# Performance work log

Hardware: AMD Instinct MI355X
Metric: run time of the kernel (lower is better)

The kernel has to match this reference:

```python
import jax, jax.numpy as jnp
import numpy as np

B, D, E, K = 8192, 1024, 8, 5  # batch, in_dim, num_size_classes, num_depth_classes
H = max(64, D)                 # hidden = max(64, in_dim)
EPS = 1e-8


def ordinal_logits_to_probs(logits, num_classes):
    # logits: [B, K-1] cumulative ordinal logits -> [B, K] class probs
    q = jax.nn.sigmoid(logits)
    probs = jnp.concatenate(
        [1.0 - q[:, :1], q[:, :-1] - q[:, 1:], q[:, -1:]], axis=1
    )  # [B, K]
    probs = jnp.clip(probs, EPS)
    return probs / jnp.clip(probs.sum(axis=1, keepdims=True), EPS)


def setup_inputs() -> dict:
    key = jax.random.key(0)
    kx, ks, k1, k2 = jax.random.split(key, 4)
    x = jax.random.normal(kx, (B, D), dtype=jnp.float32)
    size_idx = jax.random.randint(ks, (B,), 0, E, dtype=jnp.int64)
    # per-expert 2-layer MLP params: Linear(D,H) -> ReLU -> Linear(H,K-1)
    W1 = jax.random.normal(k1, (E, D, H), dtype=jnp.float32) / np.sqrt(D)
    b1 = jnp.zeros((E, H), dtype=jnp.float32)
    W2 = jax.random.normal(k2, (E, H, K - 1), dtype=jnp.float32) / np.sqrt(H)
    b2 = jnp.zeros((E, K - 1), dtype=jnp.float32)
    return {"x": x, "size_idx": size_idx, "W1": W1, "b1": b1, "W2": W2, "b2": b2}


def reference(x, size_idx, W1, b1, W2, b2):
    # Hard routing: each token gets the output of expert size_idx[b].
    # Dense all-expert compute + per-token select (same math as mask/gather/scatter,
    # dropout is inference-mode identity).
    h = jax.nn.relu(jnp.einsum('bd,edh->beh', x, W1) + b1)      # [B, E, H]
    all_logits = jnp.einsum('beh,ehk->bek', h, W2) + b2          # [B, E, K-1]
    idx = size_idx.astype(jnp.int32)[:, None, None]              # [B, 1, 1]
    logits = jnp.take_along_axis(all_logits, idx, axis=1)[:, 0]  # [B, K-1]
    probs = ordinal_logits_to_probs(logits, K)                   # [B, K]
    return logits, probs
```

## Files before the change

### kernel.cpp

```cpp
#include <hip/hip_runtime.h>
#include <cstdint>
#include <cstddef>

#define Bn 8192
#define Dn 1024
#define Hn 1024
#define En 8
#define MT 128
#define MTILES (PERM_N / MT)
#define PERM_N (Bn + En * MT)
#define NB 16

#define NXB 4096
#define NWB 2048
#define XB0 1
#define WB0 (XB0 + NXB)
#define TOTB (WB0 + NWB)

typedef unsigned short u16;
typedef __bf16 bf16x8 __attribute__((ext_vector_type(8)));
typedef float f32x4 __attribute__((ext_vector_type(4)));
typedef unsigned short ushort8 __attribute__((ext_vector_type(8)));

__device__ __forceinline__ u16 f2bf(float f) {
  unsigned int u = __float_as_uint(f);
  unsigned int r = u + 0x7fffu + ((u >> 16) & 1u);
  return (u16)(r >> 16);
}

__device__ __forceinline__ void gld16(const void* g, void* l) {
  __builtin_amdgcn_global_load_lds(
      (const __attribute__((address_space(1))) void*)g,
      (__attribute__((address_space(3))) void*)l, 16, 0, 0);
}

#define PIPE_BARRIER_VM8() do {                    \
    asm volatile("" ::: "memory");                 \
    __builtin_amdgcn_s_waitcnt(0x0F78);            \
    __builtin_amdgcn_s_barrier();                  \
    asm volatile("" ::: "memory");                 \
  } while (0)
#define PIPE_BARRIER_VM4() do {                    \
    asm volatile("" ::: "memory");                 \
    __builtin_amdgcn_s_waitcnt(0x0F74);            \
    __builtin_amdgcn_s_barrier();                  \
    asm volatile("" ::: "memory");                 \
  } while (0)
#define PIPE_BARRIER_VM0() do {                    \
    asm volatile("" ::: "memory");                 \
    __builtin_amdgcn_s_waitcnt(0x0F70);            \
    __builtin_amdgcn_s_barrier();                  \
    asm volatile("" ::: "memory");                 \
  } while (0)

__global__ __launch_bounds__(256) void prep_k(
    const float* __restrict__ x, const int* __restrict__ sidx,
    const float* __restrict__ W1,
    u16* __restrict__ xb, u16* __restrict__ w1t,
    int* __restrict__ off, int* __restrict__ perm) {
  int bid = blockIdx.x;
  int t = threadIdx.x;

  if (bid == 0) {
    __shared__ int hist[4][En];
    __shared__ int base[4][En];
    __shared__ int eoff[En + 1];
    int wv = t >> 6;
    if (t < 4 * En) ((int*)hist)[t] = 0;
#pragma unroll
    for (int i = 0; i < PERM_N / 256; i++) perm[t + i * 256] = -1;
    __syncthreads();
    int e32[32], r32[32];
#pragma unroll
    for (int i = 0; i < 32; i++) {
      int e = sidx[t + i * 256];
      e32[i] = e;
      r32[i] = atomicAdd(&hist[wv][e], 1);
    }
    __syncthreads();
    if (t < En) {
      int s = 0;
      for (int w = 0; w < 4; w++) { base[w][t] = s; s += hist[w][t]; }
      hist[0][t] = s;
    }
    __syncthreads();
    if (t == 0) {
      int o = 0;
      for (int e = 0; e < En; e++) {
        eoff[e] = o; off[e] = o;
        o += (hist[0][e] + MT - 1) & ~(MT - 1);
      }
      eoff[En] = o; off[En] = o;
    }
    __syncthreads();
#pragma unroll
    for (int i = 0; i < 32; i++) {
      int e = e32[i];
      perm[eoff[e] + base[wv][e] + r32[i]] = t + i * 256;
    }
  } else if (bid < WB0) {
    size_t idx = ((size_t)(bid - XB0) * 256 + t) * 8;
    const float* src = x + idx;
    float4 a = *(const float4*)src;
    float4 b = *(const float4*)(src + 4);
    ushort8 o;
    o[0] = f2bf(a.x); o[1] = f2bf(a.y); o[2] = f2bf(a.z); o[3] = f2bf(a.w);
    o[4] = f2bf(b.x); o[5] = f2bf(b.y); o[6] = f2bf(b.z); o[7] = f2bf(b.w);
    *(ushort8*)(xb + idx) = o;
  } else {
    __shared__ float tile[64][65];
    int wb = bid - WB0;
    int e = wb >> 8;
    int k0 = ((wb >> 4) & 15) * 64;
    int n0 = (wb & 15) * 64;
    int c4 = (t & 15) * 4;
    int r0 = t >> 4;
    const float* src = W1 + ((size_t)e << 20) + (size_t)k0 * Hn + n0;
#pragma unroll
    for (int i = 0; i < 4; i++) {
      int r = r0 + i * 16;
      float4 v = *(const float4*)(src + (size_t)r * Hn + c4);
      tile[r][c4 + 0] = v.x; tile[r][c4 + 1] = v.y;
      tile[r][c4 + 2] = v.z; tile[r][c4 + 3] = v.w;
    }
    __syncthreads();
    int kb = t & 7;
    int h0 = t >> 3;
    u16* dstE = w1t + ((size_t)e << 20);
#pragma unroll
    for (int i = 0; i < 2; i++) {
      int hl = h0 + i * 32;
      int gh = n0 + hl;
      ushort8 o;
#pragma unroll
      for (int j = 0; j < 8; j++) o[j] = f2bf(tile[kb * 8 + j][hl]);
      *(ushort8*)(dstE + (size_t)gh * Dn + k0 + kb * 8) = o;
    }
  }
}

__global__ __launch_bounds__(256) void gemm_k(
    const u16* __restrict__ xb, const u16* __restrict__ w1t,
    const float* __restrict__ b1, const float* __restrict__ w2,
    const int* __restrict__ off, const int* __restrict__ perm,
    float* __restrict__ partials) {
  __shared__ u16 As[4][4096];
  __shared__ u16 Bs[4][4096];

  int n0 = blockIdx.x * 128;
  int row0 = blockIdx.y * MT;
  if (row0 >= off[En]) return;
  int e = 0;
  while (row0 >= off[e + 1]) e++;

  int tid = threadIdx.x;
  int lane = tid & 63, w = tid >> 6;
  int wm = w >> 1, wn = w & 1;

  int srow = lane >> 2;
  int slot = lane & 3;
  int scol = (slot ^ ((srow >> 1) & 3)) * 8;
  const u16* aG[2]; const u16* bG[2];
  int lOff[2];
#pragma unroll
  for (int j = 0; j < 2; j++) {
    int rl = 32 * w + 16 * j + srow;
    int tok = perm[row0 + rl];
    if (tok < 0) tok = 0;
    aG[j] = xb + ((size_t)tok << 10) + scol;
    bG[j] = w1t + ((size_t)e << 20) + (size_t)(n0 + rl) * Dn + scol;
    lOff[j] = (32 * w + 16 * j) * 32;
  }

  f32x4 acc[4][4];
#pragma unroll
  for (int i = 0; i < 4; i++)
#pragma unroll
    for (int j = 0; j < 4; j++)
      acc[i][j] = (f32x4){0.f, 0.f, 0.f, 0.f};

  int fr = lane & 15;
  int qf = lane >> 4;
  int qs = (qf ^ ((fr >> 1) & 3)) * 8;
  int offA[4], offB[4];
#pragma unroll
  for (int i = 0; i < 4; i++)
    offA[i] = (wm * 64 + i * 16 + fr) * 32 + qs;
#pragma unroll
  for (int j = 0; j < 4; j++)
    offB[j] = (wn * 64 + j * 16 + fr) * 32 + qs;

#define ISSUE_STAGE(st) do {                                          \
    int _s = (st) & 3;                                                \
    int _ko = (st) * 32;                                              \
    gld16(aG[0] + _ko, (u16*)As[_s] + lOff[0]);                       \
    gld16(aG[1] + _ko, (u16*)As[_s] + lOff[1]);                       \
    gld16(bG[0] + _ko, (u16*)Bs[_s] + lOff[0]);                       \
    gld16(bG[1] + _ko, (u16*)Bs[_s] + lOff[1]);                       \
  } while (0)

#define COMPUTE_STAGE(st) do {                                        \
    const u16* Ab = (const u16*)As[(st) & 3];                         \
    const u16* Bb = (const u16*)Bs[(st) & 3];                         \
    bf16x8 af[4], bfr[4];                                             \
    _Pragma("unroll")                                                 \
    for (int ii = 0; ii < 4; ii++) af[ii] = *(const bf16x8*)(Ab + offA[ii]); \
    _Pragma("unroll")                                                 \
    for (int jj = 0; jj < 4; jj++) bfr[jj] = *(const bf16x8*)(Bb + offB[jj]); \
    _Pragma("unroll")                                                 \
    for (int ii = 0; ii < 4; ii++)                                    \
      _Pragma("unroll")                                               \
      for (int jj = 0; jj < 4; jj++)                                  \
        acc[ii][jj] = __builtin_amdgcn_mfma_f32_16x16x32_bf16(af[ii], bfr[jj], acc[ii][jj], 0, 0, 0); \
  } while (0)

  ISSUE_STAGE(0);
  ISSUE_STAGE(1);
  ISSUE_STAGE(2);

#pragma unroll
  for (int i = 0; i < 30; i++) {
    PIPE_BARRIER_VM8();
    if (i + 3 < 32) ISSUE_STAGE(i + 3);
    COMPUTE_STAGE(i);
  }
  PIPE_BARRIER_VM4();
  COMPUTE_STAGE(30);
  PIPE_BARRIER_VM0();
  COMPUTE_STAGE(31);

#undef ISSUE_STAGE
#undef COMPUTE_STAGE

  int fq = lane >> 4;
  float4 w2v[4]; float b1v[4];
#pragma unroll
  for (int j = 0; j < 4; j++) {
    int col = n0 + wn * 64 + j * 16 + fr;
    w2v[j] = *(const float4*)(w2 + ((size_t)e * Hn + col) * 4);
    b1v[j] = b1[(size_t)e * Hn + col];
  }
  int chunk = blockIdx.x * 2 + wn;
#pragma unroll
  for (int i = 0; i < 4; i++) {
    int rbase = wm * 64 + i * 16 + fq * 4;
#pragma unroll
    for (int r = 0; r < 4; r++) {
      float s0 = 0.f, s1 = 0.f, s2 = 0.f, s3 = 0.f;
#pragma unroll
      for (int j = 0; j < 4; j++) {
        float h = acc[i][j][r] + b1v[j];
        h = fmaxf(h, 0.f);
        s0 = fmaf(h, w2v[j].x, s0);
        s1 = fmaf(h, w2v[j].y, s1);
        s2 = fmaf(h, w2v[j].z, s2);
        s3 = fmaf(h, w2v[j].w, s3);
      }
#pragma unroll
      for (int m = 1; m < 16; m <<= 1) {
        s0 += __shfl_xor(s0, m);
        s1 += __shfl_xor(s1, m);
        s2 += __shfl_xor(s2, m);
        s3 += __shfl_xor(s3, m);
      }
      if (fr == 0) {
        int row = row0 + rbase + r;
        *(float4*)(partials + ((size_t)row * NB + chunk) * 4) =
            make_float4(s0, s1, s2, s3);
      }
    }
  }
}

__global__ void probs_k(const float* __restrict__ partials,
                        const int* __restrict__ perm, const int* __restrict__ off,
                        const int* __restrict__ sidx, const float* __restrict__ b2,
                        float* __restrict__ out) {
  int p = blockIdx.x * blockDim.x + threadIdx.x;
  if (p >= off[En]) return;
  int tok = perm[p];
  if (tok < 0) return;
  int e = sidx[tok];
  float s0 = 0.f, s1 = 0.f, s2 = 0.f, s3 = 0.f;
#pragma unroll
  for (int nb = 0; nb < NB; nb++) {
    float4 v = *(const float4*)(partials + ((size_t)p * NB + nb) * 4);
    s0 += v.x; s1 += v.y; s2 += v.z; s3 += v.w;
  }
  float l0 = s0 + b2[e * 4 + 0];
  float l1 = s1 + b2[e * 4 + 1];
  float l2 = s2 + b2[e * 4 + 2];
  float l3 = s3 + b2[e * 4 + 3];
  out[tok * 4 + 0] = l0; out[tok * 4 + 1] = l1;
  out[tok * 4 + 2] = l2; out[tok * 4 + 3] = l3;
  float q0 = 1.f / (1.f + expf(-l0));
  float q1 = 1.f / (1.f + expf(-l1));
  float q2 = 1.f / (1.f + expf(-l2));
  float q3 = 1.f / (1.f + expf(-l3));
  const float eps = 1e-8f;
  float p0 = fmaxf(1.f - q0, eps);
  float p1 = fmaxf(q0 - q1, eps);
  float p2 = fmaxf(q1 - q2, eps);
  float p3 = fmaxf(q2 - q3, eps);
  float p4 = fmaxf(q3, eps);
  float s = p0 + p1 + p2 + p3 + p4;
  float inv = 1.f / fmaxf(s, eps);
  float* pr = out + (size_t)Bn * 4 + (size_t)tok * 5;
  pr[0] = p0 * inv; pr[1] = p1 * inv; pr[2] = p2 * inv;
  pr[3] = p3 * inv; pr[4] = p4 * inv;
}

extern "C" void kernel_launch(void* const* d_in, const int* in_sizes, int n_in,
                              void* d_out, int out_size, void* d_ws, size_t ws_size,
                              hipStream_t stream) {
  const float* x  = (const float*)d_in[0];
  const int* sidx = (const int*)d_in[1];
  const float* W1 = (const float*)d_in[2];
  const float* b1 = (const float*)d_in[3];
  const float* W2 = (const float*)d_in[4];
  const float* b2 = (const float*)d_in[5];
  float* out = (float*)d_out;

  uint8_t* w = (uint8_t*)d_ws;
  int* off  = (int*)(w + 64);
  int* perm = (int*)(w + 512);
  u16* xb      = (u16*)(w + 40960);
  u16* w1t     = (u16*)(w + 40960 + 16777216);
  float* parts = (float*)(w + 40960 + 2 * 16777216);

  prep_k<<<TOTB, 256, 0, stream>>>(x, sidx, W1, xb, w1t, off, perm);
  gemm_k<<<dim3(Hn / 128, MTILES), 256, 0, stream>>>(xb, w1t, b1, W2, off, perm, parts);
  probs_k<<<(PERM_N + 255) / 256, 256, 0, stream>>>(parts, perm, off, sidx, b2, out);
}
```

Measured before the change: 175.4 us.

## Fuse x bf16 conversion into GEMM A-tile loads with register-staged double buffering

```diff
diff --git a/kernel.cpp b/kernel.cpp
--- a/kernel.cpp
+++ b/kernel.cpp
@@ -7,15 +7,10 @@
 #define Hn 1024
 #define En 8
 #define MT 128
+#define PERM_N (Bn + En * MT)
 #define MTILES (PERM_N / MT)
-#define PERM_N (Bn + En * MT)
 #define NB 16
-
-#define NXB 4096
 #define NWB 2048
-#define XB0 1
-#define WB0 (XB0 + NXB)
-#define TOTB (WB0 + NWB)
 
 typedef unsigned short u16;
 typedef __bf16 bf16x8 __attribute__((ext_vector_type(8)));
@@ -34,30 +29,9 @@
       (__attribute__((address_space(3))) void*)l, 16, 0, 0);
 }
 
-#define PIPE_BARRIER_VM8() do {                    \
-    asm volatile("" ::: "memory");                 \
-    __builtin_amdgcn_s_waitcnt(0x0F78);            \
-    __builtin_amdgcn_s_barrier();                  \
-    asm volatile("" ::: "memory");                 \
-  } while (0)
-#define PIPE_BARRIER_VM4() do {                    \
-    asm volatile("" ::: "memory");                 \
-    __builtin_amdgcn_s_waitcnt(0x0F74);            \
-    __builtin_amdgcn_s_barrier();                  \
-    asm volatile("" ::: "memory");                 \
-  } while (0)
-#define PIPE_BARRIER_VM0() do {                    \
-    asm volatile("" ::: "memory");                 \
-    __builtin_amdgcn_s_waitcnt(0x0F70);            \
-    __builtin_amdgcn_s_barrier();                  \
-    asm volatile("" ::: "memory");                 \
-  } while (0)
-
 __global__ __launch_bounds__(256) void prep_k(
-    const float* __restrict__ x, const int* __restrict__ sidx,
-    const float* __restrict__ W1,
-    u16* __restrict__ xb, u16* __restrict__ w1t,
-    int* __restrict__ off, int* __restrict__ perm) {
+    const int* __restrict__ sidx, const float* __restrict__ W1,
+    u16* __restrict__ w1t, int* __restrict__ off, int* __restrict__ perm) {
   int bid = blockIdx.x;
   int t = threadIdx.x;
 
@@ -98,18 +72,9 @@
       int e = e32[i];
       perm[eoff[e] + base[wv][e] + r32[i]] = t + i * 256;
     }
-  } else if (bid < WB0) {
-    size_t idx = ((size_t)(bid - XB0) * 256 + t) * 8;
-    const float* src = x + idx;
-    float4 a = *(const float4*)src;
-    float4 b = *(const float4*)(src + 4);
-    ushort8 o;
-    o[0] = f2bf(a.x); o[1] = f2bf(a.y); o[2] = f2bf(a.z); o[3] = f2bf(a.w);
-    o[4] = f2bf(b.x); o[5] = f2bf(b.y); o[6] = f2bf(b.z); o[7] = f2bf(b.w);
-    *(ushort8*)(xb + idx) = o;
   } else {
     __shared__ float tile[64][65];
-    int wb = bid - WB0;
+    int wb = bid - 1;
     int e = wb >> 8;
     int k0 = ((wb >> 4) & 15) * 64;
     int n0 = (wb & 15) * 64;
@@ -124,28 +89,27 @@
       tile[r][c4 + 2] = v.z; tile[r][c4 + 3] = v.w;
     }
     __syncthreads();
-    int kb = t & 7;
-    int h0 = t >> 3;
-    u16* dstE = w1t + ((size_t)e << 20);
-#pragma unroll
-    for (int i = 0; i < 2; i++) {
-      int hl = h0 + i * 32;
-      int gh = n0 + hl;
-      ushort8 o;
-#pragma unroll
-      for (int j = 0; j < 8; j++) o[j] = f2bf(tile[kb * 8 + j][hl]);
-      *(ushort8*)(dstE + (size_t)gh * Dn + k0 + kb * 8) = o;
+    u16* dst = w1t + ((size_t)e << 20) + (size_t)n0 * Dn + k0;
+#pragma unroll
+    for (int i = 0; i < 4; i++) {
+      int h = r0 + i * 16;
+      ushort4 o;
+      o.x = f2bf(tile[c4 + 0][h]);
+      o.y = f2bf(tile[c4 + 1][h]);
+      o.z = f2bf(tile[c4 + 2][h]);
+      o.w = f2bf(tile[c4 + 3][h]);
+      *(ushort4*)(dst + (size_t)h * Dn + c4) = o;
     }
   }
 }
 
 __global__ __launch_bounds__(256) void gemm_k(
-    const u16* __restrict__ xb, const u16* __restrict__ w1t,
+    const float* __restrict__ x, const u16* __restrict__ w1t,
     const float* __restrict__ b1, const float* __restrict__ w2,
     const int* __restrict__ off, const int* __restrict__ perm,
     float* __restrict__ partials) {
-  __shared__ u16 As[4][4096];
-  __shared__ u16 Bs[4][4096];
+  __shared__ u16 As[2][4096];
+  __shared__ u16 Bs[2][4096];
 
   int n0 = blockIdx.x * 128;
   int row0 = blockIdx.y * MT;
@@ -160,16 +124,19 @@
   int srow = lane >> 2;
   int slot = lane & 3;
   int scol = (slot ^ ((srow >> 1) & 3)) * 8;
-  const u16* aG[2]; const u16* bG[2];
+  const float* aF[2];
+  const u16* bG[2];
   int lOff[2];
+  int aW[2];
 #pragma unroll
   for (int j = 0; j < 2; j++) {
     int rl = 32 * w + 16 * j + srow;
     int tok = perm[row0 + rl];
     if (tok < 0) tok = 0;
-    aG[j] = xb + ((size_t)tok << 10) + scol;
+    aF[j] = x + ((size_t)tok << 10) + scol;
     bG[j] = w1t + ((size_t)e << 20) + (size_t)(n0 + rl) * Dn + scol;
     lOff[j] = (32 * w + 16 * j) * 32;
+    aW[j] = lOff[j] + lane * 8;
   }
 
   f32x4 acc[4][4];
@@ -190,18 +157,41 @@
   for (int j = 0; j < 4; j++)
     offB[j] = (wn * 64 + j * 16 + fr) * 32 + qs;
 
-#define ISSUE_STAGE(st) do {                                          \
-    int _s = (st) & 3;                                                \
+  float4 av0, av1, av2, av3;
+
+#define LOAD_A(st) do {                                               \
     int _ko = (st) * 32;                                              \
-    gld16(aG[0] + _ko, (u16*)As[_s] + lOff[0]);                       \
-    gld16(aG[1] + _ko, (u16*)As[_s] + lOff[1]);                       \
+    av0 = *(const float4*)(aF[0] + _ko);                              \
+    av1 = *(const float4*)(aF[0] + _ko + 4);                          \
+    av2 = *(const float4*)(aF[1] + _ko);                              \
+    av3 = *(const float4*)(aF[1] + _ko + 4);                          \
+  } while (0)
+
+#define WRITE_A(st) do {                                              \
+    int _s = (st) & 1;                                                \
+    ushort8 o;                                                        \
+    o[0] = f2bf(av0.x); o[1] = f2bf(av0.y);                           \
+    o[2] = f2bf(av0.z); o[3] = f2bf(av0.w);                           \
+    o[4] = f2bf(av1.x); o[5] = f2bf(av1.y);                           \
+    o[6] = f2bf(av1.z); o[7] = f2bf(av1.w);                           \
+    *(ushort8*)((u16*)As[_s] + aW[0]) = o;                            \
+    o[0] = f2bf(av2.x); o[1] = f2bf(av2.y);                           \
+    o[2] = f2bf(av2.z); o[3] = f2bf(av2.w);                           \
+    o[4] = f2bf(av3.x); o[5] = f2bf(av3.y);                           \
+    o[6] = f2bf(av3.z); o[7] = f2bf(av3.w);                           \
+    *(ushort8*)((u16*)As[_s] + aW[1]) = o;                            \
+  } while (0)
+
+#define STAGE_B(st) do {                                              \
+    int _s = (st) & 1;                                                \
+    int _ko = (st) * 32;                                              \
     gld16(bG[0] + _ko, (u16*)Bs[_s] + lOff[0]);                       \
     gld16(bG[1] + _ko, (u16*)Bs[_s] + lOff[1]);                       \
   } while (0)
 
-#define COMPUTE_STAGE(st) do {                                        \
-    const u16* Ab = (const u16*)As[(st) & 3];                         \
-    const u16* Bb = (const u16*)Bs[(st) & 3];                         \
+#define COMPUTE(st) do {                                              \
+    const u16* Ab = (const u16*)As[(st) & 1];                         \
+    const u16* Bb = (const u16*)Bs[(st) & 1];                         \
     bf16x8 af[4], bfr[4];                                             \
     _Pragma("unroll")                                                 \
     for (int ii = 0; ii < 4; ii++) af[ii] = *(const bf16x8*)(Ab + offA[ii]); \
@@ -214,23 +204,27 @@
         acc[ii][jj] = __builtin_amdgcn_mfma_f32_16x16x32_bf16(af[ii], bfr[jj], acc[ii][jj], 0, 0, 0); \
   } while (0)
 
-  ISSUE_STAGE(0);
-  ISSUE_STAGE(1);
-  ISSUE_STAGE(2);
-
-#pragma unroll
-  for (int i = 0; i < 30; i++) {
-    PIPE_BARRIER_VM8();
-    if (i + 3 < 32) ISSUE_STAGE(i + 3);
-    COMPUTE_STAGE(i);
-  }
-  PIPE_BARRIER_VM4();
-  COMPUTE_STAGE(30);
-  PIPE_BARRIER_VM0();
-  COMPUTE_STAGE(31);
-
-#undef ISSUE_STAGE
-#undef COMPUTE_STAGE
+  LOAD_A(0);
+  STAGE_B(0);
+  WRITE_A(0);
+  LOAD_A(1);
+  __syncthreads();
+
+#pragma unroll
+  for (int i = 0; i < 32; i++) {
+    if (i + 1 < 32) {
+      STAGE_B(i + 1);
+      WRITE_A(i + 1);
+      if (i + 2 < 32) LOAD_A(i + 2);
+    }
+    COMPUTE(i);
+    if (i + 1 < 32) __syncthreads();
+  }
+
+#undef LOAD_A
+#undef WRITE_A
+#undef STAGE_B
+#undef COMPUTE
 
   int fq = lane >> 4;
   float4 w2v[4]; float b1v[4];
@@ -324,11 +318,10 @@
   uint8_t* w = (uint8_t*)d_ws;
   int* off  = (int*)(w + 64);
   int* perm = (int*)(w + 512);
-  u16* xb      = (u16*)(w + 40960);
-  u16* w1t     = (u16*)(w + 40960 + 16777216);
-  float* parts = (float*)(w + 40960 + 2 * 16777216);
-
-  prep_k<<<TOTB, 256, 0, stream>>>(x, sidx, W1, xb, w1t, off, perm);
-  gemm_k<<<dim3(Hn / 128, MTILES), 256, 0, stream>>>(xb, w1t, b1, W2, off, perm, parts);
+  u16* w1t     = (u16*)(w + 40960);
+  float* parts = (float*)(w + 40960 + 16777216);
+
+  prep_k<<<1 + NWB, 256, 0, stream>>>(sidx, W1, w1t, off, perm);
+  gemm_k<<<dim3(Hn / 128, MTILES), 256, 0, stream>>>(x, w1t, b1, W2, off, perm, parts);
   probs_k<<<(PERM_N + 255) / 256, 256, 0, stream>>>(parts, perm, off, sidx, b2, out);
 }
```

New measurement: 176.7 us. About the same (+0.7%).
